# Optimization experiments

Hardware: AMD Instinct MI355X
Metric: run time of the kernel (lower is better)

## Reference

```python
import jax, jax.numpy as jnp
import numpy as np

B, S, D, H = 2, 2048, 1024, 16
DK = D // H


def setup_inputs() -> dict:
    key = jax.random.key(0)
    ks = jax.random.split(key, 12)
    sc = 1.0 / np.sqrt(D)
    inp = {
        'q': jax.random.normal(ks[0], (B, S, D), jnp.float32),
        'k': jax.random.normal(ks[1], (B, S, D), jnp.float32),
        'v': jax.random.normal(ks[2], (B, S, D), jnp.float32),
        'mask': jnp.tril(jnp.ones((S, S), jnp.int32))[None, None],  # causal [1,1,S,S]
        'w_q': jax.random.normal(ks[3], (D, D), jnp.float32) * sc,
        'b_q': jnp.zeros((D,), jnp.float32),
        'w_k': jax.random.normal(ks[4], (D, D), jnp.float32) * sc,
        'b_k': jnp.zeros((D,), jnp.float32),
        'w_v': jax.random.normal(ks[5], (D, D), jnp.float32) * sc,
        'b_v': jnp.zeros((D,), jnp.float32),
        'w_o': jax.random.normal(ks[6], (D, D), jnp.float32) * sc,
        'b_o': jnp.zeros((D,), jnp.float32),
    }
    return inp


def _split_heads(x):
    # [B,S,D] -> [B,H,S,DK]
    b, s, _ = x.shape
    return x.reshape(b, s, H, DK).transpose(0, 2, 1, 3)


def reference(q, k, v, mask, w_q, b_q, w_k, b_k, w_v, b_v, w_o, b_o):
    # Linear projections (torch Linear: x @ W.T + b)
    qh = _split_heads(q @ w_q.T + b_q)
    kh = _split_heads(k @ w_k.T + b_k)
    vh = _split_heads(v @ w_v.T + b_v)
    scores = jnp.einsum('bhqd,bhkd->bhqk', qh, kh) / jnp.sqrt(jnp.float32(DK))
    scores = jnp.where(mask == 0, jnp.float32(-1e9), scores)
    probs = jax.nn.softmax(scores, axis=-1)
    # dropout is identity in eval mode
    ctx = jnp.einsum('bhqk,bhkd->bhqd', probs, vh)  # [B,H,S,DK]
    ctx = ctx.transpose(0, 2, 1, 3).reshape(q.shape[0], -1, D)
    out = ctx @ w_o.T + b_o
    return out, probs
```

## Files before the change

### kernel.cpp

```cpp
#include <hip/hip_runtime.h>

typedef float f32x4 __attribute__((ext_vector_type(4)));
typedef short s16x8 __attribute__((ext_vector_type(8)));

#define MFMA(a, b, c) __builtin_amdgcn_mfma_f32_16x16x32_bf16((a), (b), (c), 0, 0, 0)

static __device__ __forceinline__ short f2bf(float f) {
  union { float ff; unsigned u; } v; v.ff = f;
  unsigned r = v.u + 0x7FFFu + ((v.u >> 16) & 1u);
  return (short)(r >> 16);
}

typedef __attribute__((address_space(3))) void lds_void_t;
typedef const __attribute__((address_space(1))) void gmem_void_t;
static __device__ __forceinline__ void gload_lds16(const void* g, void* l) {
  __builtin_amdgcn_global_load_lds((gmem_void_t*)g, (lds_void_t*)l, 16, 0, 0);
}

__global__ __launch_bounds__(256) void cvt_qkv_kernel(
    const float* __restrict__ q, const float* __restrict__ k, const float* __restrict__ v,
    short* __restrict__ qo, short* __restrict__ ko, short* __restrict__ vo) {
  const int y = blockIdx.y;
  const float* s = (y == 0) ? q : (y == 1) ? k : v;
  short* d = (y == 0) ? qo : (y == 1) ? ko : vo;
  const int i = blockIdx.x * 256 + threadIdx.x;
  const f32x4* s4 = (const f32x4*)s;
  f32x4 a = s4[2 * i], b = s4[2 * i + 1];
  s16x8 o;
  o[0] = f2bf(a[0]); o[1] = f2bf(a[1]); o[2] = f2bf(a[2]); o[3] = f2bf(a[3]);
  o[4] = f2bf(b[0]); o[5] = f2bf(b[1]); o[6] = f2bf(b[2]); o[7] = f2bf(b[3]);
  ((s16x8*)d)[i] = o;
}

__global__ __launch_bounds__(256) void cvt_w_kernel(
    const float* __restrict__ w0, const float* __restrict__ w1,
    const float* __restrict__ w2, const float* __restrict__ w3,
    short* __restrict__ o0, short* __restrict__ o1,
    short* __restrict__ o2, short* __restrict__ o3) {
  const int y = blockIdx.y;
  const float* s = (y == 0) ? w0 : (y == 1) ? w1 : (y == 2) ? w2 : w3;
  short* d = (y == 0) ? o0 : (y == 1) ? o1 : (y == 2) ? o2 : o3;
  const int i = blockIdx.x * 256 + threadIdx.x;
  const f32x4* s4 = (const f32x4*)s;
  f32x4 a = s4[2 * i], b = s4[2 * i + 1];
  s16x8 o;
  o[0] = f2bf(a[0]); o[1] = f2bf(a[1]); o[2] = f2bf(a[2]); o[3] = f2bf(a[3]);
  o[4] = f2bf(b[0]); o[5] = f2bf(b[1]); o[6] = f2bf(b[2]); o[7] = f2bf(b[3]);
  ((s16x8*)d)[i] = o;
}

template <int MODE>
__global__ __launch_bounds__(256) void gemm_bt_kernel(
    const short* __restrict__ A, const short* __restrict__ Bt,
    const float* __restrict__ bias, void* __restrict__ outp) {
  __shared__ short As[4096];
  __shared__ short Bs[4096];
  const int t = threadIdx.x;
  const int lane = t & 63, wave = t >> 6;
  const int wr = wave >> 1, wc = wave & 1;
  const int lr = lane & 15, lg = lane >> 4;
  const int mBase = blockIdx.x * 128, nBase = blockIdx.y * 128;

  const int rowA = t >> 2, kcA = (t & 3) << 3;
  const short* gA = A + (size_t)(mBase + rowA) * 1024 + kcA;
  const short* gB = Bt + (size_t)(nBase + rowA) * 1024 + kcA;

  f32x4 acc[4][4] = {};

  for (int k0 = 0; k0 < 1024; k0 += 32) {
    __syncthreads();
    gload_lds16(gA + k0, &As[t * 8]);
    gload_lds16(gA + 64 * 1024 + k0, &As[2048 + t * 8]);
    gload_lds16(gB + k0, &Bs[t * 8]);
    gload_lds16(gB + 64 * 1024 + k0, &Bs[2048 + t * 8]);
    __syncthreads();
    const s16x8* Av = (const s16x8*)As;
    const s16x8* Bv = (const s16x8*)Bs;
    s16x8 af[4], bfr[4];
#pragma unroll
    for (int m = 0; m < 4; ++m) af[m] = Av[(wr * 64 + m * 16 + lr) * 4 + lg];
#pragma unroll
    for (int n = 0; n < 4; ++n) bfr[n] = Bv[(wc * 64 + n * 16 + lr) * 4 + lg];
#pragma unroll
    for (int m = 0; m < 4; ++m)
#pragma unroll
      for (int n = 0; n < 4; ++n)
        acc[m][n] = MFMA(af[m], bfr[n], acc[m][n]);
  }

  const int row0 = mBase + wr * 64 + lg * 4;
  const int col0 = nBase + wc * 64 + lr;
#pragma unroll
  for (int n = 0; n < 4; ++n) {
    const int col = col0 + n * 16;
    const float bv = bias[col];
#pragma unroll
    for (int m = 0; m < 4; ++m) {
#pragma unroll
      for (int j = 0; j < 4; ++j) {
        const int r = row0 + m * 16 + j;
        const float val = acc[m][n][j] + bv;
        if (MODE == 0) {
          short* o = (short*)outp;
          const int bb = r >> 11, ss = r & 2047, hh = col >> 6, dd = col & 63;
          o[((size_t)(bb * 16 + hh) * 2048 + ss) * 64 + dd] = f2bf(val);
        } else {
          ((float*)outp)[(size_t)r * 1024 + col] = val;
        }
      }
    }
  }
}

__global__ __launch_bounds__(256) void attn_kernel(
    const short* __restrict__ Qh, const short* __restrict__ Kh,
    const short* __restrict__ Vh, float* __restrict__ probs,
    short* __restrict__ ctxo) {
  __shared__ short Ks[4096];
  __shared__ short Vt[4096];
  __shared__ short Pl[4096];
  const int t = threadIdx.x;
  const int lane = t & 63, w = t >> 6;
  const int lr = lane & 15, lg = lane >> 4;
  const int qblk = blockIdx.x, bh = blockIdx.y;
  const size_t hb = (size_t)bh * (2048 * 64);
  const int qBase = qblk * 64;

  const short* Kg = Kh + hb;
  const short* Vg = Vh + hb;

  const int qrow = qBase + w * 16 + lr;
  const s16x8 qf0 = *(const s16x8*)(Qh + hb + (size_t)qrow * 64 + lg * 8);
  const s16x8 qf1 = *(const s16x8*)(Qh + hb + (size_t)qrow * 64 + 32 + lg * 8);

  const int vkey = lane;
  const int vdkb = w * 16;
  const int x = lr & 7;

  float rs[4] = {0.f, 0.f, 0.f, 0.f};
  for (int kt = 0; kt <= qblk; ++kt) {
    const int kBase = kt * 64;
    __syncthreads();
    {
      int c = t, key = c >> 3, slot = c & 7;
      gload_lds16(Kg + (size_t)(kBase + key) * 64 + ((slot ^ (key & 7)) << 3), &Ks[c * 8]);
      c = t + 256; key = c >> 3; slot = c & 7;
      gload_lds16(Kg + (size_t)(kBase + key) * 64 + ((slot ^ (key & 7)) << 3), &Ks[c * 8]);
    }
    __syncthreads();
    const s16x8* Kv = (const s16x8*)Ks;
#pragma unroll
    for (int sub = 0; sub < 4; ++sub) {
      const int key = sub * 16 + lr;
      s16x8 kf0 = Kv[key * 8 + (lg ^ x)];
      s16x8 kf1 = Kv[key * 8 + ((lg + 4) ^ x)];
      f32x4 z = {0.f, 0.f, 0.f, 0.f};
      f32x4 sa = MFMA(qf0, kf0, z);
      sa = MFMA(qf1, kf1, sa);
      const int keyg = kBase + key;
#pragma unroll
      for (int j = 0; j < 4; ++j) {
        const int qg = qBase + w * 16 + lg * 4 + j;
        const float p = (keyg <= qg) ? __expf(sa[j] * 0.125f) : 0.f;
        rs[j] += p;
      }
    }
  }
#pragma unroll
  for (int j = 0; j < 4; ++j) {
    float vsum = rs[j];
    vsum += __shfl_xor(vsum, 1);
    vsum += __shfl_xor(vsum, 2);
    vsum += __shfl_xor(vsum, 4);
    vsum += __shfl_xor(vsum, 8);
    rs[j] = 1.f / vsum;
  }

  f32x4 cacc[4] = {};
  for (int kt = 0; kt < 32; ++kt) {
    const int kBase = kt * 64;
    if (kt <= qblk) {
      __syncthreads();
      {
        int c = t, key = c >> 3, slot = c & 7;
        gload_lds16(Kg + (size_t)(kBase + key) * 64 + ((slot ^ (key & 7)) << 3), &Ks[c * 8]);
        c = t + 256; key = c >> 3; slot = c & 7;
        gload_lds16(Kg + (size_t)(kBase + key) * 64 + ((slot ^ (key & 7)) << 3), &Ks[c * 8]);
      }
      const s16x8* vsrc = (const s16x8*)(Vg + (size_t)(kBase + vkey) * 64 + vdkb);
      const s16x8 v0 = vsrc[0], v1 = vsrc[1];
#pragma unroll
      for (int i = 0; i < 8; ++i) {
        const int r0 = vdkb + i, r1 = vdkb + 8 + i;
        Vt[r0 * 64 + (vkey ^ ((r0 & 7) << 3))] = v0[i];
        Vt[r1 * 64 + (vkey ^ ((r1 & 7) << 3))] = v1[i];
      }
      __syncthreads();
      const s16x8* Kv = (const s16x8*)Ks;
#pragma unroll
      for (int sub = 0; sub < 4; ++sub) {
        const int key = sub * 16 + lr;
        s16x8 kf0 = Kv[key * 8 + (lg ^ x)];
        s16x8 kf1 = Kv[key * 8 + ((lg + 4) ^ x)];
        f32x4 z = {0.f, 0.f, 0.f, 0.f};
        f32x4 sa = MFMA(qf0, kf0, z);
        sa = MFMA(qf1, kf1, sa);
        const int keyg = kBase + key;
#pragma unroll
        for (int j = 0; j < 4; ++j) {
          const int qq = lg * 4 + j;
          const int qg = qBase + w * 16 + qq;
          const float p = (keyg <= qg) ? __expf(sa[j] * 0.125f) * rs[j] : 0.f;
          probs[(size_t)(bh * 2048 + qg) * 2048 + keyg] = p;
          Pl[w * 1024 + qq * 64 + (key ^ ((qq & 7) << 3))] = f2bf(p);
        }
      }
      const s16x8* Pv = (const s16x8*)Pl;
      const s16x8* Vv = (const s16x8*)Vt;
      s16x8 pf0 = Pv[w * 128 + lr * 8 + (lg ^ x)];
      s16x8 pf1 = Pv[w * 128 + lr * 8 + ((lg + 4) ^ x)];
#pragma unroll
      for (int n = 0; n < 4; ++n) {
        const int row = n * 16 + lr;
        s16x8 vf0 = Vv[row * 8 + (lg ^ x)];
        s16x8 vf1 = Vv[row * 8 + ((lg + 4) ^ x)];
        cacc[n] = MFMA(pf0, vf0, cacc[n]);
        cacc[n] = MFMA(pf1, vf1, cacc[n]);
      }
    } else {
#pragma unroll
      for (int sub = 0; sub < 4; ++sub) {
#pragma unroll
        for (int j = 0; j < 4; ++j) {
          const int qg = qBase + w * 16 + lg * 4 + j;
          probs[(size_t)(bh * 2048 + qg) * 2048 + kBase + sub * 16 + lr] = 0.f;
        }
      }
    }
  }

  const int bb = bh >> 4, hh = bh & 15;
#pragma unroll
  for (int n = 0; n < 4; ++n) {
    const int dcol = hh * 64 + n * 16 + lr;
#pragma unroll
    for (int j = 0; j < 4; ++j) {
      const int srow = qBase + w * 16 + lg * 4 + j;
      ctxo[(size_t)(bb * 2048 + srow) * 1024 + dcol] = f2bf(cacc[n][j]);
    }
  }
}

extern "C" void kernel_launch(void* const* d_in, const int* in_sizes, int n_in,
                              void* d_out, int out_size, void* d_ws, size_t ws_size,
                              hipStream_t stream) {
  const float* q  = (const float*)d_in[0];
  const float* k  = (const float*)d_in[1];
  const float* v  = (const float*)d_in[2];
  const float* wq = (const float*)d_in[4];
  const float* bq = (const float*)d_in[5];
  const float* wk = (const float*)d_in[6];
  const float* bk = (const float*)d_in[7];
  const float* wv = (const float*)d_in[8];
  const float* bv = (const float*)d_in[9];
  const float* wo = (const float*)d_in[10];
  const float* bo = (const float*)d_in[11];

  char* ws = (char*)d_ws;
  const size_t MB = 1u << 20;
  short* qb  = (short*)(ws);
  short* kb  = (short*)(ws + 8 * MB);
  short* vb  = (short*)(ws + 16 * MB);
  short* wqb = (short*)(ws + 24 * MB);
  short* wkb = (short*)(ws + 26 * MB);
  short* wvb = (short*)(ws + 28 * MB);
  short* wob = (short*)(ws + 30 * MB);
  short* Qh  = (short*)(ws + 32 * MB);
  short* Kh  = (short*)(ws + 40 * MB);
  short* Vh  = (short*)(ws + 48 * MB);
  short* ctx = (short*)(ws + 56 * MB);

  float* outp  = (float*)d_out;
  float* probs = outp + (size_t)4096 * 1024;

  cvt_qkv_kernel<<<dim3(2048, 3), 256, 0, stream>>>(q, k, v, qb, kb, vb);
  cvt_w_kernel<<<dim3(512, 4), 256, 0, stream>>>(wq, wk, wv, wo, wqb, wkb, wvb, wob);

  dim3 gg(32, 8);
  gemm_bt_kernel<0><<<gg, 256, 0, stream>>>(qb, wqb, bq, Qh);
  gemm_bt_kernel<0><<<gg, 256, 0, stream>>>(kb, wkb, bk, Kh);
  gemm_bt_kernel<0><<<gg, 256, 0, stream>>>(vb, wvb, bv, Vh);

  attn_kernel<<<dim3(32, 32), 256, 0, stream>>>(Qh, Kh, Vh, probs, ctx);

  gemm_bt_kernel<1><<<gg, 256, 0, stream>>>(ctx, wob, bo, outp);
}
```

Measured before the change: 837.0 us.

## Transpose score MFMA for vectorized probs stores, batch QKV GEMMs, narrow O tile

The attention kernel swaps the MFMA operand order so each lane holds four consecutive keys of a single query row. This turns the probs writes and the masked-zero writes into 16-byte vector stores, simplifies the row-sum reduction, and makes P writes to LDS 8-byte vectors. The three QKV projection GEMMs are merged into one launch over a z dimension. The output GEMM uses a 128x64 tile so it launches 512 blocks instead of 256, which should fill more CUs at the cost of reloading A tiles more often.

```diff
diff --git a/kernel.cpp b/kernel.cpp
--- a/kernel.cpp
+++ b/kernel.cpp
@@ -2,6 +2,7 @@
 
 typedef float f32x4 __attribute__((ext_vector_type(4)));
 typedef short s16x8 __attribute__((ext_vector_type(8)));
+typedef short s16x4 __attribute__((ext_vector_type(4)));
 
 #define MFMA(a, b, c) __builtin_amdgcn_mfma_f32_16x16x32_bf16((a), (b), (c), 0, 0, 0)
 
@@ -49,49 +50,50 @@
   ((s16x8*)d)[i] = o;
 }
 
-template <int MODE>
-__global__ __launch_bounds__(256) void gemm_bt_kernel(
+template <int MODE, int NFRAG>
+static __device__ __forceinline__ void gemm_body(
     const short* __restrict__ A, const short* __restrict__ Bt,
     const float* __restrict__ bias, void* __restrict__ outp) {
+  constexpr int BN = NFRAG * 32;
   __shared__ short As[4096];
-  __shared__ short Bs[4096];
+  __shared__ short Bs[BN * 32];
   const int t = threadIdx.x;
   const int lane = t & 63, wave = t >> 6;
   const int wr = wave >> 1, wc = wave & 1;
   const int lr = lane & 15, lg = lane >> 4;
-  const int mBase = blockIdx.x * 128, nBase = blockIdx.y * 128;
+  const int mBase = blockIdx.x * 128, nBase = blockIdx.y * BN;
 
   const int rowA = t >> 2, kcA = (t & 3) << 3;
   const short* gA = A + (size_t)(mBase + rowA) * 1024 + kcA;
   const short* gB = Bt + (size_t)(nBase + rowA) * 1024 + kcA;
 
-  f32x4 acc[4][4] = {};
+  f32x4 acc[4][NFRAG] = {};
 
   for (int k0 = 0; k0 < 1024; k0 += 32) {
     __syncthreads();
     gload_lds16(gA + k0, &As[t * 8]);
     gload_lds16(gA + 64 * 1024 + k0, &As[2048 + t * 8]);
     gload_lds16(gB + k0, &Bs[t * 8]);
-    gload_lds16(gB + 64 * 1024 + k0, &Bs[2048 + t * 8]);
+    if constexpr (NFRAG == 4) gload_lds16(gB + 64 * 1024 + k0, &Bs[2048 + t * 8]);
     __syncthreads();
     const s16x8* Av = (const s16x8*)As;
     const s16x8* Bv = (const s16x8*)Bs;
-    s16x8 af[4], bfr[4];
+    s16x8 af[4], bfr[NFRAG];
 #pragma unroll
     for (int m = 0; m < 4; ++m) af[m] = Av[(wr * 64 + m * 16 + lr) * 4 + lg];
 #pragma unroll
-    for (int n = 0; n < 4; ++n) bfr[n] = Bv[(wc * 64 + n * 16 + lr) * 4 + lg];
+    for (int n = 0; n < NFRAG; ++n) bfr[n] = Bv[(wc * NFRAG * 16 + n * 16 + lr) * 4 + lg];
 #pragma unroll
     for (int m = 0; m < 4; ++m)
 #pragma unroll
-      for (int n = 0; n < 4; ++n)
+      for (int n = 0; n < NFRAG; ++n)
         acc[m][n] = MFMA(af[m], bfr[n], acc[m][n]);
   }
 
   const int row0 = mBase + wr * 64 + lg * 4;
-  const int col0 = nBase + wc * 64 + lr;
-#pragma unroll
-  for (int n = 0; n < 4; ++n) {
+  const int col0 = nBase + wc * NFRAG * 16 + lr;
+#pragma unroll
+  for (int n = 0; n < NFRAG; ++n) {
     const int col = col0 + n * 16;
     const float bv = bias[col];
 #pragma unroll
@@ -110,6 +112,25 @@
       }
     }
   }
+}
+
+__global__ __launch_bounds__(256) void gemm_qkv_kernel(
+    const short* __restrict__ qb, const short* __restrict__ kb, const short* __restrict__ vb,
+    const short* __restrict__ wqb, const short* __restrict__ wkb, const short* __restrict__ wvb,
+    const float* __restrict__ bq, const float* __restrict__ bk, const float* __restrict__ bv,
+    short* __restrict__ Qh, short* __restrict__ Kh, short* __restrict__ Vh) {
+  const int z = blockIdx.z;
+  const short* A  = (z == 0) ? qb : (z == 1) ? kb : vb;
+  const short* Bt = (z == 0) ? wqb : (z == 1) ? wkb : wvb;
+  const float* bias = (z == 0) ? bq : (z == 1) ? bk : bv;
+  short* out = (z == 0) ? Qh : (z == 1) ? Kh : Vh;
+  gemm_body<0, 4>(A, Bt, bias, out);
+}
+
+__global__ __launch_bounds__(256) void gemm_o_kernel(
+    const short* __restrict__ A, const short* __restrict__ Bt,
+    const float* __restrict__ bias, float* __restrict__ outp) {
+  gemm_body<1, 2>(A, Bt, bias, outp);
 }
 
 __global__ __launch_bounds__(256) void attn_kernel(
@@ -129,15 +150,16 @@
   const short* Kg = Kh + hb;
   const short* Vg = Vh + hb;
 
-  const int qrow = qBase + w * 16 + lr;
-  const s16x8 qf0 = *(const s16x8*)(Qh + hb + (size_t)qrow * 64 + lg * 8);
-  const s16x8 qf1 = *(const s16x8*)(Qh + hb + (size_t)qrow * 64 + 32 + lg * 8);
+  const int qg = qBase + w * 16 + lr;
+  const s16x8 qf0 = *(const s16x8*)(Qh + hb + (size_t)qg * 64 + lg * 8);
+  const s16x8 qf1 = *(const s16x8*)(Qh + hb + (size_t)qg * 64 + 32 + lg * 8);
 
   const int vkey = lane;
   const int vdkb = w * 16;
   const int x = lr & 7;
-
-  float rs[4] = {0.f, 0.f, 0.f, 0.f};
+  const int px = (lr & 7) << 3;
+
+  float rs = 0.f;
   for (int kt = 0; kt <= qblk; ++kt) {
     const int kBase = kt * 64;
     __syncthreads();
@@ -155,26 +177,17 @@
       s16x8 kf0 = Kv[key * 8 + (lg ^ x)];
       s16x8 kf1 = Kv[key * 8 + ((lg + 4) ^ x)];
       f32x4 z = {0.f, 0.f, 0.f, 0.f};
-      f32x4 sa = MFMA(qf0, kf0, z);
-      sa = MFMA(qf1, kf1, sa);
-      const int keyg = kBase + key;
-#pragma unroll
-      for (int j = 0; j < 4; ++j) {
-        const int qg = qBase + w * 16 + lg * 4 + j;
-        const float p = (keyg <= qg) ? __expf(sa[j] * 0.125f) : 0.f;
-        rs[j] += p;
-      }
-    }
-  }
-#pragma unroll
-  for (int j = 0; j < 4; ++j) {
-    float vsum = rs[j];
-    vsum += __shfl_xor(vsum, 1);
-    vsum += __shfl_xor(vsum, 2);
-    vsum += __shfl_xor(vsum, 4);
-    vsum += __shfl_xor(vsum, 8);
-    rs[j] = 1.f / vsum;
-  }
+      f32x4 sa = MFMA(kf0, qf0, z);
+      sa = MFMA(kf1, qf1, sa);
+      const int key0 = kBase + sub * 16 + lg * 4;
+#pragma unroll
+      for (int j = 0; j < 4; ++j)
+        if (key0 + j <= qg) rs += __expf(sa[j] * 0.125f);
+    }
+  }
+  rs += __shfl_xor(rs, 16);
+  rs += __shfl_xor(rs, 32);
+  const float rinv = 1.f / rs;
 
   f32x4 cacc[4] = {};
   for (int kt = 0; kt < 32; ++kt) {
@@ -203,22 +216,22 @@
         s16x8 kf0 = Kv[key * 8 + (lg ^ x)];
         s16x8 kf1 = Kv[key * 8 + ((lg + 4) ^ x)];
         f32x4 z = {0.f, 0.f, 0.f, 0.f};
-        f32x4 sa = MFMA(qf0, kf0, z);
-        sa = MFMA(qf1, kf1, sa);
-        const int keyg = kBase + key;
-#pragma unroll
-        for (int j = 0; j < 4; ++j) {
-          const int qq = lg * 4 + j;
-          const int qg = qBase + w * 16 + qq;
-          const float p = (keyg <= qg) ? __expf(sa[j] * 0.125f) * rs[j] : 0.f;
-          probs[(size_t)(bh * 2048 + qg) * 2048 + keyg] = p;
-          Pl[w * 1024 + qq * 64 + (key ^ ((qq & 7) << 3))] = f2bf(p);
-        }
-      }
-      const s16x8* Pv = (const s16x8*)Pl;
+        f32x4 sa = MFMA(kf0, qf0, z);
+        sa = MFMA(kf1, qf1, sa);
+        const int key0 = kBase + sub * 16 + lg * 4;
+        f32x4 p4;
+#pragma unroll
+        for (int j = 0; j < 4; ++j)
+          p4[j] = (key0 + j <= qg) ? __expf(sa[j] * 0.125f) * rinv : 0.f;
+        *(f32x4*)&probs[(size_t)(bh * 2048 + qg) * 2048 + key0] = p4;
+        s16x4 pb;
+        pb[0] = f2bf(p4[0]); pb[1] = f2bf(p4[1]);
+        pb[2] = f2bf(p4[2]); pb[3] = f2bf(p4[3]);
+        *(s16x4*)&Pl[w * 1024 + lr * 64 + ((sub * 16 + lg * 4) ^ px)] = pb;
+      }
       const s16x8* Vv = (const s16x8*)Vt;
-      s16x8 pf0 = Pv[w * 128 + lr * 8 + (lg ^ x)];
-      s16x8 pf1 = Pv[w * 128 + lr * 8 + ((lg + 4) ^ x)];
+      const s16x8 pf0 = *(const s16x8*)&Pl[w * 1024 + lr * 64 + ((lg * 8) ^ px)];
+      const s16x8 pf1 = *(const s16x8*)&Pl[w * 1024 + lr * 64 + ((32 + lg * 8) ^ px)];
 #pragma unroll
       for (int n = 0; n < 4; ++n) {
         const int row = n * 16 + lr;
@@ -228,13 +241,11 @@
         cacc[n] = MFMA(pf1, vf1, cacc[n]);
       }
     } else {
-#pragma unroll
-      for (int sub = 0; sub < 4; ++sub) {
-#pragma unroll
-        for (int j = 0; j < 4; ++j) {
-          const int qg = qBase + w * 16 + lg * 4 + j;
-          probs[(size_t)(bh * 2048 + qg) * 2048 + kBase + sub * 16 + lr] = 0.f;
-        }
+      const f32x4 zz = {0.f, 0.f, 0.f, 0.f};
+#pragma unroll
+      for (int i = 0; i < 4; ++i) {
+        const int row = qBase + w * 16 + i * 4 + lg;
+        *(f32x4*)&probs[(size_t)(bh * 2048 + row) * 2048 + kBase + lr * 4] = zz;
       }
     }
   }
@@ -286,12 +297,10 @@
   cvt_qkv_kernel<<<dim3(2048, 3), 256, 0, stream>>>(q, k, v, qb, kb, vb);
   cvt_w_kernel<<<dim3(512, 4), 256, 0, stream>>>(wq, wk, wv, wo, wqb, wkb, wvb, wob);
 
-  dim3 gg(32, 8);
-  gemm_bt_kernel<0><<<gg, 256, 0, stream>>>(qb, wqb, bq, Qh);
-  gemm_bt_kernel<0><<<gg, 256, 0, stream>>>(kb, wkb, bk, Kh);
-  gemm_bt_kernel<0><<<gg, 256, 0, stream>>>(vb, wvb, bv, Vh);
+  gemm_qkv_kernel<<<dim3(32, 8, 3), 256, 0, stream>>>(
+      qb, kb, vb, wqb, wkb, wvb, bq, bk, bv, Qh, Kh, Vh);
 
   attn_kernel<<<dim3(32, 32), 256, 0, stream>>>(Qh, Kh, Vh, probs, ctx);
 
-  gemm_bt_kernel<1><<<gg, 256, 0, stream>>>(ctx, wob, bo, outp);
-}
+  gemm_o_kernel<<<dim3(32, 16), 256, 0, stream>>>(ctx, wob, bo, outp);
+}
```

New measurement: 768.5 us. 1.09x faster.
